# Performance work log

Hardware: AMD Instinct MI355X
Metric: run time of the kernel (lower is better)

Reference implementation:

```python
import jax, jax.numpy as jnp
import numpy as np

SR = 16000            # radiance_sampling_rate
GAMMA = 1e-3          # fsm_gamma
NUM_BOUNCES = 8
N_PATCHES = 256
N_RAD = 24000         # num_radiances
NNZ = 480000
L = 1600              # echogram_len = SR * 0.1
N_FREQ_CHUNKS = 9     # 801 = 9 * 89; chunk spmm over frequency to bound memory


def setup_inputs() -> dict:
    key = jax.random.key(0)
    ks = jax.random.split(key, 10)
    return {
        "absorption_coefficient": jax.random.uniform(ks[0], (N_PATCHES,), jnp.float32),
        "scattering_coefficient": jax.random.uniform(ks[1], (2, N_PATCHES), jnp.float32),
        "initial_radiance": jax.random.uniform(ks[2], (N_RAD, L), jnp.float32),
        "detection_weights": jax.random.uniform(ks[3], (N_RAD,), jnp.float32),
        "envelope": jnp.zeros((L,), jnp.float32),
        "sparse_kernel_basis": jax.random.uniform(ks[4], (2, NNZ), jnp.float32),
        "sparse_kernel_row": jax.random.randint(ks[5], (NNZ,), 0, N_RAD, jnp.int32),
        "sparse_kernel_col": jax.random.randint(ks[6], (NNZ,), 0, N_RAD, jnp.int32),
        "sparse_kernel_reflector_id": jax.random.randint(ks[7], (NNZ,), 0, N_PATCHES, jnp.int32),
        "delay_samples": jax.random.randint(ks[8], (N_RAD,), 0, 1500, jnp.int32),
    }


def _spmm(vals, row, col, X, n_seg, n_chunks):
    """COO sparse [n_seg,n_seg] @ dense [n_seg,F], chunked over F."""
    N, F = X.shape
    Xc = jnp.moveaxis(X.reshape(N, n_chunks, F // n_chunks), 1, 0)  # [C,N,f]
    def body(_, xc):
        contrib = vals[:, None] * xc[col]                 # gather [nnz,f]
        return None, jax.ops.segment_sum(contrib, row, num_segments=n_seg)
    _, Y = jax.lax.scan(body, None, Xc)
    return jnp.moveaxis(Y, 0, 1).reshape(N, F)


def reference(absorption_coefficient, scattering_coefficient, initial_radiance,
              detection_weights, envelope, sparse_kernel_basis,
              sparse_kernel_row, sparse_kernel_col, sparse_kernel_reflector_id,
              delay_samples):
    log_gamma = jnp.log(jnp.float32(GAMMA))
    t = jnp.arange(L, dtype=jnp.float32) / SR
    fsm = jnp.exp(log_gamma * t)                          # fsm_window [L]

    # ---- compose_kernel: gather per-patch coefficients onto nnz entries ----
    a = absorption_coefficient[sparse_kernel_reflector_id]        # [nnz]
    s = scattering_coefficient[:, sparse_kernel_reflector_id]     # [2,nnz]
    vals = (s * sparse_kernel_basis).sum(0) * a                   # [nnz]

    # ---- fsm-corrected frequency-domain main ART loop ----
    R0 = jnp.fft.rfft(initial_radiance * fsm[None, :], axis=-1)   # [N,F] complex
    d = delay_samples.astype(jnp.float32)
    k = jnp.arange(L // 2 + 1, dtype=jnp.float32)
    # rfft of fsm-weighted integer delay impulse: fsm[d] * exp(-2pi i k d / L)
    D = (jnp.exp(log_gamma * d / SR)[:, None]
         * jnp.exp(-2j * jnp.pi * d[:, None] * k[None, :] / L))    # [N,F]
    vals_c = vals.astype(R0.dtype)

    def bounce(carry, _):
        cur, total = carry
        cur = _spmm(vals_c, sparse_kernel_row, sparse_kernel_col,
                    cur * D, N_RAD, N_FREQ_CHUNKS)
        return (cur, total + cur), None

    (_, total), _ = jax.lax.scan(bounce, (R0, R0), None, length=NUM_BOUNCES)
    radiance = jnp.fft.irfft(total, n=L, axis=-1) / fsm[None, :]   # undo fsm

    # ---- detection + learnable envelope ----
    echogram = detection_weights @ radiance                        # [L]
    echogram = echogram * jnp.exp(envelope)
    return echogram
```

## Files before the change

kernel.cpp:

```cpp
#include <hip/hip_runtime.h>
#include <hip/hip_fp16.h>
#include <math.h>


static constexpr float kSR = 16000.0f;
static constexpr int   kL = 1600;
static constexpr int   kNRad = 24000;
static constexpr int   kNNZ = 480000;
static constexpr int   kNPatch = 256;
static constexpr int   kNBounce = 8;
static constexpr int   kSW = 64;
static constexpr int   kNS = 25;
static constexpr int   kNRB = 750;
static constexpr float kLogGamma = -6.907755278982137f;

__device__ __forceinline__ unsigned short f2bf(float f) {
    unsigned int u = __float_as_uint(f);
    unsigned int r = u + 0x7fffu + ((u >> 16) & 1u);
    return (unsigned short)(r >> 16);
}
__device__ __forceinline__ float bflo(unsigned int w) {
    return __uint_as_float(w << 16);
}
__device__ __forceinline__ float bfhi(unsigned int w) {
    return __uint_as_float(w & 0xffff0000u);
}
__device__ __forceinline__ void fma8(float (&a)[8], float v, const uint4 q) {
    a[0] = fmaf(v, bflo(q.x), a[0]);
    a[1] = fmaf(v, bfhi(q.x), a[1]);
    a[2] = fmaf(v, bflo(q.y), a[2]);
    a[3] = fmaf(v, bfhi(q.y), a[3]);
    a[4] = fmaf(v, bflo(q.z), a[4]);
    a[5] = fmaf(v, bfhi(q.z), a[5]);
    a[6] = fmaf(v, bflo(q.w), a[6]);
    a[7] = fmaf(v, bfhi(q.w), a[7]);
}


__global__ void k_hist(const int* __restrict__ row, int* __restrict__ cnt) {
    int e = blockIdx.x * 256 + threadIdx.x;
    if (e < kNNZ) atomicAdd(&cnt[row[e]], 1);
}

__global__ void k_deghist(const int* __restrict__ cnt, int* __restrict__ degcnt) {
    int i = blockIdx.x * 256 + threadIdx.x;
    if (i < kNRad) atomicAdd(&degcnt[min(cnt[i], 63)], 1);
}

__global__ void k_degscan(int* __restrict__ degcnt, int* __restrict__ degcur) {
    if (threadIdx.x == 0) {
        int s = 0;
        for (int b = 0; b < 64; ++b) {
            int c = degcnt[b];
            degcnt[b] = s;
            degcur[b] = s;
            s += c;
        }
    }
}

__global__ void k_perm(const int* __restrict__ cnt, int* __restrict__ degcur,
                       int* __restrict__ perm, int* __restrict__ iperm) {
    int i = blockIdx.x * 256 + threadIdx.x;
    if (i >= kNRad) return;
    int b = min(cnt[i], 63);
    int pos = atomicAdd(&degcur[b], 1);
    perm[pos] = i;
    iperm[i] = pos;
}

__global__ void k_scan2(const int* __restrict__ cnt, const int* __restrict__ perm,
                        int* __restrict__ rowptr, int* __restrict__ cursor) {
    __shared__ int s[256];
    __shared__ int carry_s;
    int tid = threadIdx.x;
    if (tid == 0) carry_s = 0;
    __syncthreads();
    for (int base = 0; base < kNRad; base += 256) {
        int i = base + tid;
        int v = (i < kNRad) ? cnt[perm[i]] : 0;
        s[tid] = v;
        __syncthreads();
        for (int off = 1; off < 256; off <<= 1) {
            int t = (tid >= off) ? s[tid - off] : 0;
            __syncthreads();
            s[tid] += t;
            __syncthreads();
        }
        int incl = s[tid];
        int c = carry_s;
        if (i < kNRad) {
            int ex = c + incl - v;
            rowptr[i] = ex;
            cursor[i] = ex;
        }
        __syncthreads();
        if (tid == 255) carry_s = c + incl;
        __syncthreads();
    }
    if (tid == 0) rowptr[kNRad] = carry_s;
}

__global__ void k_scatter(const float* __restrict__ absorb,
                          const float* __restrict__ scat,
                          const float* __restrict__ basis,
                          const int* __restrict__ row,
                          const int* __restrict__ col,
                          const int* __restrict__ rid,
                          const int* __restrict__ iperm,
                          int* __restrict__ cursor,
                          unsigned int* __restrict__ epack) {
    int e = blockIdx.x * 256 + threadIdx.x;
    if (e >= kNNZ) return;
    int rd = rid[e];
    float v = (scat[rd] * basis[e] + scat[kNPatch + rd] * basis[kNNZ + e]) * absorb[rd];
    int p = iperm[row[e]];
    int pos = atomicAdd(&cursor[p], 1);
    unsigned int hv = (unsigned int)__half_as_ushort(__float2half(v));
    epack[pos] = (hv << 16) | (unsigned int)col[e];
}

__global__ void k_decay(const int* __restrict__ delay,
                        float* __restrict__ decay, int* __restrict__ dmod) {
    int i = blockIdx.x * 256 + threadIdx.x;
    if (i >= kNRad) return;
    int d = delay[i];
    decay[i] = expf(kLogGamma * (float)d / kSR);
    dmod[i] = d % kL;
}


__global__ __launch_bounds__(256) void k_init(const float* __restrict__ rad,
                                              const float* __restrict__ w,
                                              const float* __restrict__ decay,
                                              const int* __restrict__ dmod,
                                              unsigned short* __restrict__ outS,
                                              float* __restrict__ ypartA) {
    int rb = blockIdx.x;
    int tid = threadIdx.x, wv = tid >> 6, lane = tid & 63;
    const size_t SS = (size_t)kNRad * kSW;
    for (int k = 0; k < kNS; ++k) {
        int m = k * kSW + lane;
        float fs = expf(kLogGamma * (float)m / kSR);
        float y = 0.0f;
#pragma unroll
        for (int g = 0; g < 8; ++g) {
            int r = rb * 32 + wv * 8 + g;
            float v = rad[(size_t)r * kL + m] * fs;
            y = fmaf(w[r], v, y);
            int n = m + dmod[r];
            if (n >= kL) n -= kL;
            outS[(size_t)(n >> 6) * SS + (size_t)r * kSW + (n & 63)] =
                f2bf(decay[r] * v);
        }
        ypartA[((size_t)(rb * 4 + wv)) * kL + m] = y;
    }
}


__global__ __launch_bounds__(256) void k_bounce(const unsigned short* __restrict__ inS,
                                                unsigned short* __restrict__ outS,
                                                float* __restrict__ ypart,
                                                const unsigned int* __restrict__ epack,
                                                const int* __restrict__ rowptr,
                                                const int* __restrict__ perm,
                                                const float* __restrict__ w,
                                                const float* __restrict__ decay,
                                                const int* __restrict__ dmod) {
    int bid = blockIdx.x;
    int x = bid & 7;
    int rb = bid >> 3;
    int tid = threadIdx.x, wv = tid >> 6, lane = tid & 63;
    int g = lane >> 3, p = lane & 7;
    int r = rb * 32 + wv * 8 + g;
    int e0 = rowptr[r], e1 = rowptr[r + 1];
    bool own24 = ((rb & 7) == x);
    const size_t SS = (size_t)kNRad * kSW;
    const unsigned short* b0 = inS + (size_t)x * SS + (size_t)p * 8;
    const unsigned short* b3 = inS + (size_t)24 * SS + (size_t)p * 8;

    float acc0[8] = {0, 0, 0, 0, 0, 0, 0, 0};
    float acc1[8] = {0, 0, 0, 0, 0, 0, 0, 0};
    float acc2[8] = {0, 0, 0, 0, 0, 0, 0, 0};
    float acc3[8] = {0, 0, 0, 0, 0, 0, 0, 0};

    for (int e = e0; e < e1; ++e) {
        unsigned int u = epack[e];
        float v = __half2float(__ushort_as_half((unsigned short)(u >> 16)));
        size_t co = (size_t)(u & 0xffffu) * kSW;
        uint4 q0 = *(const uint4*)(b0 + co);
        uint4 q1 = *(const uint4*)(b0 + 8 * SS + co);
        uint4 q2 = *(const uint4*)(b0 + 16 * SS + co);
        fma8(acc0, v, q0);
        fma8(acc1, v, q1);
        fma8(acc2, v, q2);
        if (own24) {
            uint4 q3 = *(const uint4*)(b3 + co);
            fma8(acc3, v, q3);
        }
    }

    __shared__ float tb[4][8][64];
    float* ypB = ypart + ((size_t)(rb * 4 + wv)) * kL;

    auto emit = [&](const float (&A)[8], int S) {
#pragma unroll
        for (int i = 0; i < 8; ++i) tb[wv][g][p * 8 + i] = A[i];
        float yk = 0.0f;
#pragma unroll
        for (int g2 = 0; g2 < 8; ++g2) {
            int o2 = perm[rb * 32 + wv * 8 + g2];
            float val = tb[wv][g2][lane];
            yk = fmaf(w[o2], val, yk);
            int n = S * kSW + lane + dmod[o2];
            if (n >= kL) n -= kL;
            if (n >= kL) n -= kL;
            outS[(size_t)(n >> 6) * SS + (size_t)o2 * kSW + (n & 63)] =
                f2bf(decay[o2] * val);
        }
        ypB[S * kSW + lane] += yk;
    };

    emit(acc0, x);
    emit(acc1, x + 8);
    emit(acc2, x + 16);
    if (own24) emit(acc3, 24);
}


__global__ void k_red1(const float* __restrict__ ypA,
                       const float* __restrict__ ypB,
                       float* __restrict__ partial) {
    int c = blockIdx.x / 7;
    int nb = blockIdx.x % 7;
    int n = nb * 256 + threadIdx.x;
    if (n >= kL) return;
    float s = 0.0f;
    int r0 = c * 125;
    for (int i = 0; i < 125; ++i) s += ypA[(size_t)(r0 + i) * kL + n];
    for (int i = 0; i < 125; ++i) s += ypB[(size_t)(r0 + i) * kL + n];
    partial[(size_t)c * kL + n] = s;
}

__global__ void k_red2(const float* __restrict__ partial,
                       const float* __restrict__ env,
                       float* __restrict__ out) {
    int n = blockIdx.x * 256 + threadIdx.x;
    if (n >= kL) return;
    float s = 0.0f;
#pragma unroll
    for (int c = 0; c < 24; ++c) s += partial[(size_t)c * kL + n];
    float t = (float)n / kSR;
    out[n] = s * expf(env[n] - kLogGamma * t);
}

extern "C" void kernel_launch(void* const* d_in, const int* in_sizes, int n_in,
                              void* d_out, int out_size, void* d_ws, size_t ws_size,
                              hipStream_t stream) {
    const float* absorb = (const float*)d_in[0];
    const float* scat   = (const float*)d_in[1];
    const float* rad    = (const float*)d_in[2];
    const float* w      = (const float*)d_in[3];
    const float* env    = (const float*)d_in[4];
    const float* basis  = (const float*)d_in[5];
    const int*   srow   = (const int*)d_in[6];
    const int*   scol   = (const int*)d_in[7];
    const int*   srid   = (const int*)d_in[8];
    const int*   delay  = (const int*)d_in[9];

    char* ws = (char*)d_ws;
    size_t off = 0;
    auto alloc = [&](size_t bytes) -> char* {
        char* p = ws + off;
        off += (bytes + 255) & ~size_t(255);
        return p;
    };
    unsigned short* curA = (unsigned short*)alloc((size_t)kNS * kNRad * kSW * 2);
    unsigned short* curB = (unsigned short*)alloc((size_t)kNS * kNRad * kSW * 2);
    float* ypartA = (float*)alloc((size_t)3000 * kL * 4);
    float* ypartB = (float*)alloc((size_t)3000 * kL * 4);
    float* partial = (float*)alloc((size_t)24 * kL * 4);
    unsigned int* epack = (unsigned int*)alloc((size_t)kNNZ * 4);
    int*   rowptr = (int*)alloc((size_t)(kNRad + 1) * 4);
    int*   cursor = (int*)alloc((size_t)kNRad * 4);
    int*   cnt    = (int*)alloc((size_t)kNRad * 4);
    int*   perm   = (int*)alloc((size_t)kNRad * 4);
    int*   iperm  = (int*)alloc((size_t)kNRad * 4);
    float* decay  = (float*)alloc((size_t)kNRad * 4);
    int*   dmod   = (int*)alloc((size_t)kNRad * 4);
    int*   degcnt = (int*)alloc(64 * 4);
    int*   degcur = (int*)alloc(64 * 4);
    (void)ws_size; (void)in_sizes; (void)n_in; (void)out_size;

    hipMemsetAsync(cnt, 0, (size_t)kNRad * 4, stream);
    hipMemsetAsync(degcnt, 0, 64 * 4, stream);
    hipMemsetAsync(ypartB, 0, (size_t)3000 * kL * 4, stream);

    k_hist<<<(kNNZ + 255) / 256, 256, 0, stream>>>(srow, cnt);
    k_deghist<<<(kNRad + 255) / 256, 256, 0, stream>>>(cnt, degcnt);
    k_degscan<<<1, 64, 0, stream>>>(degcnt, degcur);
    k_perm<<<(kNRad + 255) / 256, 256, 0, stream>>>(cnt, degcur, perm, iperm);
    k_scan2<<<1, 256, 0, stream>>>(cnt, perm, rowptr, cursor);
    k_decay<<<(kNRad + 255) / 256, 256, 0, stream>>>(delay, decay, dmod);
    k_scatter<<<(kNNZ + 255) / 256, 256, 0, stream>>>(absorb, scat, basis, srow,
                                                      scol, srid, iperm, cursor, epack);

    k_init<<<kNRB, 256, 0, stream>>>(rad, w, decay, dmod, curA, ypartA);

    const unsigned short* in = curA;
    unsigned short* outb = curB;
    for (int b = 0; b < kNBounce; ++b) {
        k_bounce<<<kNRB * 8, 256, 0, stream>>>(in, outb, ypartB, epack, rowptr,
                                               perm, w, decay, dmod);
        const unsigned short* tmp = outb;
        outb = (unsigned short*)in;
        in = tmp;
    }

    k_red1<<<24 * 7, 256, 0, stream>>>(ypartA, ypartB, partial);
    k_red2<<<(kL + 255) / 256, 256, 0, stream>>>(partial, env, (float*)d_out);
}
```

Before: 1.946 ms.

## Split bounce slices across three grid phases and unroll gather loop by four

The bounce kernel now launches three times as many blocks, each handling a single 64-sample time slice instead of three or four, so the gather of neighbour radiances is spread over more concurrent workgroups. The inner edge loop is unrolled by four so several independent 16-byte gathers are in flight at once. The init kernel is reshaped into 3000 single-wavefront blocks. In exchange, each block re-reads its row's sparse entries once per slice, and the epack/rowptr traffic grows threefold.

Result: faster. 1.646 ms (-15.4%).

```diff
diff --git a/kernel.cpp b/kernel.cpp
--- a/kernel.cpp
+++ b/kernel.cpp
@@ -24,6 +24,9 @@
 }
 __device__ __forceinline__ float bfhi(unsigned int w) {
     return __uint_as_float(w & 0xffff0000u);
+}
+__device__ __forceinline__ float h2f(unsigned int hv) {
+    return __half2float(__ushort_as_half((unsigned short)hv));
 }
 __device__ __forceinline__ void fma8(float (&a)[8], float v, const uint4 q) {
     a[0] = fmaf(v, bflo(q.x), a[0]);
@@ -130,14 +133,14 @@
 }
 
 
-__global__ __launch_bounds__(256) void k_init(const float* __restrict__ rad,
-                                              const float* __restrict__ w,
-                                              const float* __restrict__ decay,
-                                              const int* __restrict__ dmod,
-                                              unsigned short* __restrict__ outS,
-                                              float* __restrict__ ypartA) {
-    int rb = blockIdx.x;
-    int tid = threadIdx.x, wv = tid >> 6, lane = tid & 63;
+__global__ __launch_bounds__(64) void k_init(const float* __restrict__ rad,
+                                             const float* __restrict__ w,
+                                             const float* __restrict__ decay,
+                                             const int* __restrict__ dmod,
+                                             unsigned short* __restrict__ outS,
+                                             float* __restrict__ ypartA) {
+    int bid = blockIdx.x;
+    int lane = threadIdx.x;
     const size_t SS = (size_t)kNRad * kSW;
     for (int k = 0; k < kNS; ++k) {
         int m = k * kSW + lane;
@@ -145,7 +148,7 @@
         float y = 0.0f;
 #pragma unroll
         for (int g = 0; g < 8; ++g) {
-            int r = rb * 32 + wv * 8 + g;
+            int r = bid * 8 + g;
             float v = rad[(size_t)r * kL + m] * fs;
             y = fmaf(w[r], v, y);
             int n = m + dmod[r];
@@ -153,7 +156,7 @@
             outS[(size_t)(n >> 6) * SS + (size_t)r * kSW + (n & 63)] =
                 f2bf(decay[r] * v);
         }
-        ypartA[((size_t)(rb * 4 + wv)) * kL + m] = y;
+        ypartA[(size_t)bid * kL + m] = y;
     }
 }
 
@@ -169,43 +172,41 @@
                                                 const int* __restrict__ dmod) {
     int bid = blockIdx.x;
     int x = bid & 7;
-    int rb = bid >> 3;
+    int t = bid >> 3;
+    int phase = t / kNRB;
+    int rb = t - phase * kNRB;
     int tid = threadIdx.x, wv = tid >> 6, lane = tid & 63;
     int g = lane >> 3, p = lane & 7;
     int r = rb * 32 + wv * 8 + g;
     int e0 = rowptr[r], e1 = rowptr[r + 1];
-    bool own24 = ((rb & 7) == x);
     const size_t SS = (size_t)kNRad * kSW;
-    const unsigned short* b0 = inS + (size_t)x * SS + (size_t)p * 8;
-    const unsigned short* b3 = inS + (size_t)24 * SS + (size_t)p * 8;
-
-    float acc0[8] = {0, 0, 0, 0, 0, 0, 0, 0};
-    float acc1[8] = {0, 0, 0, 0, 0, 0, 0, 0};
-    float acc2[8] = {0, 0, 0, 0, 0, 0, 0, 0};
-    float acc3[8] = {0, 0, 0, 0, 0, 0, 0, 0};
-
-    for (int e = e0; e < e1; ++e) {
-        unsigned int u = epack[e];
-        float v = __half2float(__ushort_as_half((unsigned short)(u >> 16)));
-        size_t co = (size_t)(u & 0xffffu) * kSW;
-        uint4 q0 = *(const uint4*)(b0 + co);
-        uint4 q1 = *(const uint4*)(b0 + 8 * SS + co);
-        uint4 q2 = *(const uint4*)(b0 + 16 * SS + co);
-        fma8(acc0, v, q0);
-        fma8(acc1, v, q1);
-        fma8(acc2, v, q2);
-        if (own24) {
-            uint4 q3 = *(const uint4*)(b3 + co);
-            fma8(acc3, v, q3);
-        }
-    }
-
     __shared__ float tb[4][8][64];
-    float* ypB = ypart + ((size_t)(rb * 4 + wv)) * kL;
-
-    auto emit = [&](const float (&A)[8], int S) {
+
+    auto do_slice = [&](int S) {
+        const unsigned short* b = inS + (size_t)S * SS + (size_t)p * 8;
+        float acc[8] = {0, 0, 0, 0, 0, 0, 0, 0};
+        int e = e0;
+        for (; e + 4 <= e1; e += 4) {
+            unsigned int u0 = epack[e];
+            unsigned int u1 = epack[e + 1];
+            unsigned int u2 = epack[e + 2];
+            unsigned int u3 = epack[e + 3];
+            uint4 q0 = *(const uint4*)(b + (size_t)(u0 & 0xffffu) * kSW);
+            uint4 q1 = *(const uint4*)(b + (size_t)(u1 & 0xffffu) * kSW);
+            uint4 q2 = *(const uint4*)(b + (size_t)(u2 & 0xffffu) * kSW);
+            uint4 q3 = *(const uint4*)(b + (size_t)(u3 & 0xffffu) * kSW);
+            fma8(acc, h2f(u0 >> 16), q0);
+            fma8(acc, h2f(u1 >> 16), q1);
+            fma8(acc, h2f(u2 >> 16), q2);
+            fma8(acc, h2f(u3 >> 16), q3);
+        }
+        for (; e < e1; ++e) {
+            unsigned int u = epack[e];
+            uint4 q = *(const uint4*)(b + (size_t)(u & 0xffffu) * kSW);
+            fma8(acc, h2f(u >> 16), q);
+        }
 #pragma unroll
-        for (int i = 0; i < 8; ++i) tb[wv][g][p * 8 + i] = A[i];
+        for (int i = 0; i < 8; ++i) tb[wv][g][p * 8 + i] = acc[i];
         float yk = 0.0f;
 #pragma unroll
         for (int g2 = 0; g2 < 8; ++g2) {
@@ -218,13 +219,11 @@
             outS[(size_t)(n >> 6) * SS + (size_t)o2 * kSW + (n & 63)] =
                 f2bf(decay[o2] * val);
         }
-        ypB[S * kSW + lane] += yk;
+        ypart[((size_t)(rb * 4 + wv)) * kL + S * kSW + lane] += yk;
     };
 
-    emit(acc0, x);
-    emit(acc1, x + 8);
-    emit(acc2, x + 16);
-    if (own24) emit(acc3, 24);
+    do_slice(x + 8 * phase);
+    if (phase == 2 && ((rb & 7) == x)) do_slice(24);
 }
 
 
@@ -305,13 +304,13 @@
     k_scatter<<<(kNNZ + 255) / 256, 256, 0, stream>>>(absorb, scat, basis, srow,
                                                       scol, srid, iperm, cursor, epack);
 
-    k_init<<<kNRB, 256, 0, stream>>>(rad, w, decay, dmod, curA, ypartA);
+    k_init<<<3000, 64, 0, stream>>>(rad, w, decay, dmod, curA, ypartA);
 
     const unsigned short* in = curA;
     unsigned short* outb = curB;
     for (int b = 0; b < kNBounce; ++b) {
-        k_bounce<<<kNRB * 8, 256, 0, stream>>>(in, outb, ypartB, epack, rowptr,
-                                               perm, w, decay, dmod);
+        k_bounce<<<3 * kNRB * 8, 256, 0, stream>>>(in, outb, ypartB, epack, rowptr,
+                                                   perm, w, decay, dmod);
         const unsigned short* tmp = outb;
         outb = (unsigned short*)in;
         in = tmp;
```
